# Kernel optimization log

Hardware: AMD Instinct MI355X
Metric: run time of the kernel (lower is better)

## Reference

```python
import jax, jax.numpy as jnp
import numpy as np

DT = 1e-3
TAU_SYN_INV = 200.0  # norse default 1/5e-3
TAU_MEM_INV = 100.0  # norse default 1/1e-2
A_PLUS, A_MINUS = 0.004, 0.003


def conv(x, w):
    return jax.lax.conv_general_dilated(x, w, (1, 1), 'VALID',
                                        dimension_numbers=('NCHW', 'OIHW', 'NCHW'))


def maxpool(x, k, s):
    return jax.lax.reduce_window(x, -jnp.inf, jax.lax.max, (1, 1, k, k), (1, 1, s, s), 'VALID')


def iaf(v_state, inp, v_th):
    # integrate-and-fire: accumulate, spike at threshold, reset to 0
    v = v_state + inp
    z = (v >= v_th).astype(inp.dtype)
    return z, v * (1.0 - z), v  # spikes, new state, pre-reset potential


def stdp(s_pre, w, v, mask, threshold):
    # get_update_index: per-output-channel winner (max masked potential, batch-avg)
    # STDP_learning: multiplicative STDP dw = (a+*pre - a-*(1-pre)) * w * (1-w) at winner, gated by v>threshold
    C, k = w.shape[0], w.shape[-1]
    pm = jnp.mean(v * mask, axis=0)                 # [C,H,W]
    Wd = pm.shape[-1]
    flat = pm.reshape(C, -1)
    idx = jnp.argmax(flat, axis=1)
    maxval = jnp.max(flat, axis=1)
    h, ww = idx // Wd, idx % Wd
    pre = jnp.mean(s_pre, axis=0)                   # [Cin,Hp,Wp]
    patch = lambda hc, wc: jax.lax.dynamic_slice(pre, (0, hc, wc), (pre.shape[0], k, k))
    patches = jax.vmap(patch)(h, ww)                # [C,Cin,k,k]
    fired = (maxval >= threshold)[:, None, None, None]
    dw = jnp.where(fired, A_PLUS * patches - A_MINUS * (1.0 - patches), 0.0) * w * (1.0 - w)
    return jnp.clip(w + dw, 0.0, 1.0)


def setup_inputs() -> dict:
    key = jax.random.key(0)
    ks = jax.random.split(key, 8)
    T, B = 30, 32
    x = jax.random.uniform(ks[0], (T, B, 1, 240, 160), dtype=jnp.float32)
    w1 = 0.8 + 0.05 * jax.random.normal(ks[1], (4, 1, 5, 5), dtype=jnp.float32)
    w2 = 0.8 + 0.05 * jax.random.normal(ks[2], (20, 4, 16, 16), dtype=jnp.float32)
    w3 = 0.8 + 0.05 * jax.random.normal(ks[3], (10, 20, 5, 5), dtype=jnp.float32)
    fc1_w = jax.random.normal(ks[4], (50, B * 10), dtype=jnp.float32) / np.sqrt(B * 10)
    fc1_b = jnp.zeros((50,), jnp.float32)
    out_w = jax.random.normal(ks[5], (10, 50), dtype=jnp.float32) / np.sqrt(50)
    out_b = jnp.zeros((10,), jnp.float32)
    return {'x': x, 'w1': w1, 'w2': w2, 'w3': w3,
            'fc1_w': fc1_w, 'fc1_b': fc1_b, 'out_w': out_w, 'out_b': out_b}


def reference(x, w1, w2, w3, fc1_w, fc1_b, out_w, out_b):
    T, B = x.shape[0], x.shape[1]
    v1 = jnp.zeros((B, 4, 236, 156), x.dtype)
    v2 = jnp.zeros((B, 20, 24, 10), x.dtype)
    v3 = jnp.zeros((B, 10, 8, 1), x.dtype)
    m1, m2, m3 = jnp.ones_like(v1), jnp.ones_like(v2), jnp.ones_like(v3)
    lv = jnp.zeros((1, 10), x.dtype)
    li = jnp.zeros((1, 10), x.dtype)

    def step(carry, xt):
        w1, w2, w3, v1, v2, v3, m1, m2, m3, lv, li = carry
        # layer 1: conv -> IAF -> lateral inhibition (once fired, inhibited)
        z2, v1n, v1p = iaf(v1, conv(xt, w1), 10.0)
        z2 = z2 * m1; m1n = m1 * (1.0 - z2)
        z3 = maxpool(z2, 7, 6)
        z5, v2n, v2p = iaf(v2, conv(z3, w2), 60.0)
        z5 = z5 * m2; m2n = m2 * (1.0 - z5)
        z6 = maxpool(z5, 2, 2)
        z8, v3n, v3p = iaf(v3, conv(z6, w3), 2.0)
        z8 = z8 * m3; m3n = m3 * (1.0 - z8)
        z9 = jnp.max(z8, axis=(2, 3))                       # global max pool -> [B,10]
        # STDP weight updates (torch runs these under no_grad)
        w1n = jax.lax.stop_gradient(stdp(xt, w1, v1p, m1n, 10.0))
        w2n = jax.lax.stop_gradient(stdp(z3, w2, v2p, m2n, 60.0))
        w3n = jax.lax.stop_gradient(stdp(z6, w3, v3p, m3n, 2.0))
        # readout: z9.view(-1, B*10) -> [1, B*10] -> fc1 -> relu -> LILinearCell
        feat = jax.lax.stop_gradient(z9).reshape(1, -1)
        h = jax.nn.relu(feat @ fc1_w.T + fc1_b)
        i_dec = li * (1.0 - DT * TAU_SYN_INV)
        v_new = lv + DT * TAU_MEM_INV * (i_dec - lv)
        i_new = i_dec + h @ out_w.T + out_b
        volt = jnp.broadcast_to(v_new, (B, 10))
        return (w1n, w2n, w3n, v1n, v2n, v3n, m1n, m2n, m3n, v_new, i_new), volt

    carry0 = (w1, w2, w3, v1, v2, v3, m1, m2, m3, lv, li)
    carry, volts = jax.lax.scan(step, carry0, x)
    return volts, carry[0], carry[1]
```

## Files before the change

### kernel.cpp

```cpp
#include <hip/hip_runtime.h>


#define T_STEPS 30
#define BATCH   32
#define H_IN    240
#define W_IN    160
#define C1      4
#define H1      236
#define W1O     156
#define H3      39
#define W3      25
#define C2      20
#define H2      24
#define W2O     10
#define C3      10
#define H8      8

#define N1PB   (C1*H1*W1O)
#define N_V1   (BATCH*N1PB)
#define N_V2PB (C2*H2*W2O)
#define N_V2   (BATCH*N_V2PB)
#define Z3PB   (C1*H3*W3)
#define N_Z3   (BATCH*Z3PB)
#define N_POOL (BATCH*H3*W3)
#define N_FEAT (BATCH*C3)

#define NTHR 256

__device__ __forceinline__ float wave64_sum_dpp(float s) {
  s += __int_as_float(__builtin_amdgcn_update_dpp(0, __float_as_int(s), 0x111, 0xf, 0xf, true));
  s += __int_as_float(__builtin_amdgcn_update_dpp(0, __float_as_int(s), 0x112, 0xf, 0xf, true));
  s += __int_as_float(__builtin_amdgcn_update_dpp(0, __float_as_int(s), 0x114, 0xf, 0xf, true));
  s += __int_as_float(__builtin_amdgcn_update_dpp(0, __float_as_int(s), 0x118, 0xf, 0xf, true));
  s += __int_as_float(__builtin_amdgcn_update_dpp(0, __float_as_int(s), 0x142, 0xa, 0xf, true));
  s += __int_as_float(__builtin_amdgcn_update_dpp(0, __float_as_int(s), 0x143, 0xc, 0xf, true));
  return s;
}

__global__ __launch_bounds__(NTHR) void k1_conv1pool(
    const float* __restrict__ x, const float* __restrict__ w1,
    unsigned char* __restrict__ z3, int* alive_flag)
{
  __shared__ float s_w1[C1*25];
  for (int i = threadIdx.x; i < C1*25; i += NTHR) s_w1[i] = w1[i];
  __syncthreads();
  int it = blockIdx.x*NTHR + threadIdx.x;
  if (it == 0) *alive_flag = 0;
  int o = it >> 3, q = it & 7;
  int px = o % W3; int tt = o / W3;
  int py = tt % H3; int b = tt / H3;
  unsigned mask = 0;
  if (q < 7) {
    const float* xb = x + (size_t)b*H_IN*W_IN;
    int ybase = py*6 + q;
    float acc[C1][7];
    #pragma unroll
    for (int c = 0; c < C1; ++c)
      #pragma unroll
      for (int wx = 0; wx < 7; ++wx) acc[c][wx] = 0.f;
    #pragma unroll
    for (int i = 0; i < 5; ++i) {
      const float* xp = xb + (size_t)(ybase + i)*W_IN + px*6;
      float xr[11];
      #pragma unroll
      for (int k = 0; k < 11; ++k) xr[k] = xp[k];
      #pragma unroll
      for (int j = 0; j < 5; ++j) {
        float w0 = s_w1[ 0 + i*5 + j];
        float w1v = s_w1[25 + i*5 + j];
        float w2v = s_w1[50 + i*5 + j];
        float w3v = s_w1[75 + i*5 + j];
        #pragma unroll
        for (int wx = 0; wx < 7; ++wx) {
          float xv = xr[wx + j];
          acc[0][wx] = fmaf(xv, w0,  acc[0][wx]);
          acc[1][wx] = fmaf(xv, w1v, acc[1][wx]);
          acc[2][wx] = fmaf(xv, w2v, acc[2][wx]);
          acc[3][wx] = fmaf(xv, w3v, acc[3][wx]);
        }
      }
    }
    #pragma unroll
    for (int c = 0; c < C1; ++c)
      #pragma unroll
      for (int wx = 0; wx < 7; ++wx)
        mask |= (acc[c][wx] >= 10.f) ? (1u << c) : 0u;
  }
  mask |= __shfl_xor(mask, 1, 64);
  mask |= __shfl_xor(mask, 2, 64);
  mask |= __shfl_xor(mask, 4, 64);
  if (q == 0 && o < N_POOL) {
    unsigned char* zp = z3 + (size_t)b*Z3PB + py*W3 + px;
    zp[0]        =  mask       & 1;
    zp[H3*W3]    = (mask >> 1) & 1;
    zp[2*H3*W3]  = (mask >> 2) & 1;
    zp[3*H3*W3]  = (mask >> 3) & 1;
  }
}

__global__ __launch_bounds__(NTHR) void k2_conv2(
    const unsigned char* __restrict__ z3, const float* __restrict__ w2,
    unsigned char* __restrict__ z5, int* alive_flag)
{
  __shared__ unsigned s_mask[C1*H3];
  __shared__ int s_any[4];
  const int b = blockIdx.x & 31;
  const int c = blockIdx.x >> 5;
  const int tid = threadIdx.x;
  const int lane = tid & 63;
  const int wv = tid >> 6;
  if (tid < C1*H3) {
    const unsigned char* rp = z3 + (size_t)b*Z3PB + tid*W3;
    unsigned m = 0;
    #pragma unroll
    for (int k = 0; k < W3; ++k) m |= (rp[k] ? 1u : 0u) << k;
    s_mask[tid] = m;
  }
  float wreg[16];
  {
    const float4* wp = (const float4*)(w2 + (size_t)c*C1*256 + lane*16);
    #pragma unroll
    for (int k = 0; k < 4; ++k) {
      float4 v = wp[k];
      wreg[4*k+0] = v.x; wreg[4*k+1] = v.y; wreg[4*k+2] = v.z; wreg[4*k+3] = v.w;
    }
  }
  __syncthreads();
  const int mrow = (lane >> 4)*H3 + (lane & 15);
  int surv = 0;
  for (int oy = wv*6; oy < wv*6 + 6; ++oy) {
    unsigned mw = s_mask[mrow + oy];
    #pragma unroll
    for (int ox = 0; ox < 10; ++ox) {
      unsigned mm = mw >> ox;
      float s = 0.f;
      #pragma unroll
      for (int j = 0; j < 16; ++j)
        s += (mm & (1u << j)) ? wreg[j] : 0.f;
      s = wave64_sum_dpp(s);
      if (lane == 63) {
        unsigned char sp = (s >= 60.0f) ? 1 : 0;
        z5[b*N_V2PB + c*(H2*W2O) + oy*W2O + ox] = sp;
        surv |= (sp == 0);
      }
    }
  }
  if (lane == 63) s_any[wv] = surv;
  __syncthreads();
  if (tid == 0 && (s_any[0] | s_any[1] | s_any[2] | s_any[3]))
    *alive_flag = 1;
}

__global__ __launch_bounds__(NTHR) void k3_conv3(
    const unsigned char* __restrict__ z5, const float* __restrict__ w3,
    float* __restrict__ z9)
{
  const int b = blockIdx.x, tid = threadIdx.x;
  __shared__ unsigned int s_z5w[N_V2PB/4];
  __shared__ unsigned char s_z8[C3*H8];
  const unsigned int* zsrc = (const unsigned int*)(z5 + (size_t)b*N_V2PB);
  for (int i = tid; i < N_V2PB/4; i += NTHR) s_z5w[i] = zsrc[i];
  __syncthreads();
  const unsigned char* sz = (const unsigned char*)s_z5w;
  for (int it = tid; it < C3*H8*4; it += NTHR) {
    int o = it >> 2, g = it & 3;
    int c3 = o >> 3, oy = o & 7;
    float s = 0.f;
    for (int ci = g*5; ci < g*5 + 5; ++ci) {
      const unsigned char* zp = sz + ci*H2*W2O;
      const float* wp = w3 + ((size_t)c3*C2 + ci)*25;
      #pragma unroll
      for (int i = 0; i < 5; ++i) {
        const unsigned char* r0 = zp + (2*(oy + i))*W2O;
        const unsigned char* r1 = r0 + W2O;
        #pragma unroll
        for (int j = 0; j < 5; ++j) {
          unsigned char zv = r0[2*j] | r0[2*j+1] | r1[2*j] | r1[2*j+1];
          s = fmaf((float)zv, wp[i*5 + j], s);
        }
      }
    }
    s += __shfl_xor(s, 1, 64);
    s += __shfl_xor(s, 2, 64);
    if (g == 0) s_z8[o] = (s >= 2.0f) ? 1 : 0;
  }
  __syncthreads();
  if (tid < C3) {
    unsigned char r = 0;
    #pragma unroll
    for (int k = 0; k < H8; ++k) r |= s_z8[tid*H8 + k];
    z9[b*C3 + tid] = (float)r;
  }
}

__global__ __launch_bounds__(NTHR) void f1_fallback(
    const float* __restrict__ x,  const float* __restrict__ w1,
    const float* __restrict__ w2, const float* __restrict__ w3,
    float* v1, unsigned char* m1, unsigned char* z2,
    float* __restrict__ z9, const int* alive_flag)
{
  if (*alive_flag == 0) return;
  const int b = blockIdx.x, tid = threadIdx.x;
  __shared__ float s_w1[C1*25];
  __shared__ unsigned char s_z3[Z3PB];
  __shared__ float s_v2[N_V2PB];
  __shared__ unsigned char s_m2[N_V2PB], s_z5[N_V2PB];
  __shared__ float s_v3[C3*H8];
  __shared__ unsigned char s_m3[C3*H8], s_z8[C3*H8];

  for (int i = tid; i < C1*25; i += NTHR) s_w1[i] = w1[i];
  float* v1b = v1 + (size_t)b*N1PB;
  unsigned char* m1b = m1 + (size_t)b*N1PB;
  unsigned char* z2b = z2 + (size_t)b*N1PB;
  __syncthreads();

  const float* x0 = x + (size_t)b*H_IN*W_IN;
  for (int idx = tid; idx < N1PB; idx += NTHR) {
    int xw = idx % W1O; int r = idx / W1O;
    int y  = r % H1;    int c = r / H1;
    const float* xp = x0 + (size_t)y*W_IN + xw;
    const float* wp = s_w1 + c*25;
    float s = 0.f;
    #pragma unroll
    for (int i = 0; i < 5; ++i)
      #pragma unroll
      for (int j = 0; j < 5; ++j) s = fmaf(xp[i*W_IN + j], wp[i*5 + j], s);
    bool z = (s >= 10.0f);
    v1b[idx] = z ? 0.f : s;
    m1b[idx] = z ? 0 : 1;
  }
  __syncthreads();
  for (int i = tid; i < Z3PB; i += NTHR) {
    int px = i % W3; int r = i / W3;
    int py = r % H3; int cc = r / H3;
    const unsigned char* p = m1b + ((size_t)cc*H1 + py*6)*W1O + px*6;
    unsigned char rr = 0;
    #pragma unroll
    for (int ii = 0; ii < 7; ++ii)
      #pragma unroll
      for (int jj = 0; jj < 7; ++jj) rr |= (p[ii*W1O + jj] == 0) ? 1 : 0;
    s_z3[i] = rr;
  }
  __syncthreads();
  for (int o = tid; o < N_V2PB; o += NTHR) {
    int c  = o / (H2*W2O);
    int r  = o - c*(H2*W2O);
    int oy = r / W2O, ox = r - (r/W2O)*W2O;
    const float* wb = w2 + (size_t)c*C1*256;
    float s = 0.f;
    for (int ci = 0; ci < C1; ++ci)
      for (int i = 0; i < 16; ++i) {
        const unsigned char* ip = s_z3 + (ci*H3 + oy + i)*W3 + ox;
        const float* wp = wb + ci*256 + i*16;
        #pragma unroll
        for (int j = 0; j < 16; ++j) s = fmaf((float)ip[j], wp[j], s);
      }
    bool z = (s >= 60.0f);
    s_v2[o] = z ? 0.f : s;
    s_m2[o] = z ? 0 : 1;
    s_z5[o] = z ? 1 : 0;
  }
  __syncthreads();
  for (int o = tid; o < C3*H8; o += NTHR) {
    int c3 = o >> 3, oy = o & 7;
    float s = 0.f;
    for (int ci = 0; ci < C2; ++ci) {
      const unsigned char* zp = s_z5 + ci*H2*W2O;
      const float* wp = w3 + ((size_t)c3*C2 + ci)*25;
      #pragma unroll
      for (int i = 0; i < 5; ++i) {
        const unsigned char* r0 = zp + (2*(oy + i))*W2O;
        const unsigned char* r1 = r0 + W2O;
        #pragma unroll
        for (int j = 0; j < 5; ++j) {
          unsigned char zv = r0[2*j] | r0[2*j+1] | r1[2*j] | r1[2*j+1];
          s = fmaf((float)zv, wp[i*5 + j], s);
        }
      }
    }
    bool z = (s >= 2.0f);
    s_v3[o] = z ? 0.f : s;
    s_m3[o] = z ? 0 : 1;
    s_z8[o] = z ? 1 : 0;
  }
  __syncthreads();
  if (tid < C3) {
    unsigned char r = 0;
    #pragma unroll
    for (int k = 0; k < H8; ++k) r |= s_z8[tid*H8 + k];
    z9[b*C3 + tid] = (float)r;
  }
  __syncthreads();

  for (int t = 1; t < T_STEPS; ++t) {
    const float* xt = x + ((size_t)t*BATCH + b)*H_IN*W_IN;
    for (int idx = tid; idx < N1PB; idx += NTHR) {
      int xw = idx % W1O; int r = idx / W1O;
      int y  = r % H1;    int c = r / H1;
      const float* xp = xt + (size_t)y*W_IN + xw;
      const float* wp = s_w1 + c*25;
      float s = 0.f;
      #pragma unroll
      for (int i = 0; i < 5; ++i)
        #pragma unroll
        for (int j = 0; j < 5; ++j) s = fmaf(xp[i*W_IN + j], wp[i*5 + j], s);
      float v = v1b[idx] + s;
      bool  z = (v >= 10.0f);
      v1b[idx] = z ? 0.f : v;
      unsigned char m = m1b[idx];
      z2b[idx] = (z && m) ? 1 : 0;
      m1b[idx] = (m && !z) ? 1 : 0;
    }
    __syncthreads();
    for (int i = tid; i < Z3PB; i += NTHR) {
      int px = i % W3; int r = i / W3;
      int py = r % H3; int c = r / H3;
      const unsigned char* p = z2b + ((size_t)c*H1 + py*6)*W1O + px*6;
      unsigned char rr = 0;
      #pragma unroll
      for (int ii = 0; ii < 7; ++ii)
        #pragma unroll
        for (int jj = 0; jj < 7; ++jj) rr |= p[ii*W1O + jj];
      s_z3[i] = rr;
    }
    __syncthreads();
    for (int o = tid; o < N_V2PB; o += NTHR) {
      int c  = o / (H2*W2O);
      int r  = o - c*(H2*W2O);
      int oy = r / W2O, ox = r - (r/W2O)*W2O;
      const float* wb = w2 + (size_t)c*C1*256;
      float s = 0.f;
      for (int ci = 0; ci < C1; ++ci)
        for (int i = 0; i < 16; ++i) {
          const unsigned char* ip = s_z3 + (ci*H3 + oy + i)*W3 + ox;
          const float* wp = wb + ci*256 + i*16;
          #pragma unroll
          for (int j = 0; j < 16; ++j) s = fmaf((float)ip[j], wp[j], s);
        }
      float v = s_v2[o] + s;
      bool  z = (v >= 60.0f);
      s_v2[o] = z ? 0.f : v;
      unsigned char m = s_m2[o];
      s_z5[o] = (z && m) ? 1 : 0;
      s_m2[o] = (m && !z) ? 1 : 0;
    }
    __syncthreads();
    for (int o = tid; o < C3*H8; o += NTHR) {
      int c3 = o >> 3, oy = o & 7;
      float s = 0.f;
      for (int ci = 0; ci < C2; ++ci) {
        const unsigned char* zp = s_z5 + ci*H2*W2O;
        const float* wp = w3 + ((size_t)c3*C2 + ci)*25;
        #pragma unroll
        for (int i = 0; i < 5; ++i) {
          const unsigned char* r0 = zp + (2*(oy + i))*W2O;
          const unsigned char* r1 = r0 + W2O;
          #pragma unroll
          for (int j = 0; j < 5; ++j) {
            unsigned char zv = r0[2*j] | r0[2*j+1] | r1[2*j] | r1[2*j+1];
            s = fmaf((float)zv, wp[i*5 + j], s);
          }
        }
      }
      float v = s_v3[o] + s;
      bool  z = (v >= 2.0f);
      s_v3[o] = z ? 0.f : v;
      unsigned char m = s_m3[o];
      s_z8[o] = (z && m) ? 1 : 0;
      s_m3[o] = (m && !z) ? 1 : 0;
    }
    __syncthreads();
    if (tid < C3) {
      unsigned char r = 0;
      #pragma unroll
      for (int k = 0; k < H8; ++k) r |= s_z8[tid*H8 + k];
      z9[(size_t)t*N_FEAT + b*C3 + tid] = (float)r;
    }
    __syncthreads();
  }
}

__global__ __launch_bounds__(NTHR) void f2_head(
    const float* __restrict__ z9,
    const float* __restrict__ fc1_w, const float* __restrict__ fc1_b,
    const float* __restrict__ out_w, const float* __restrict__ out_b,
    const float* __restrict__ w1,    const float* __restrict__ w2,
    float* __restrict__ out, const int* alive_flag)
{
  const int tid = threadIdx.x;
  const int gid = blockIdx.x*NTHR + tid;
  const int gsz = gridDim.x*NTHR;
  float* out_w1 = out + T_STEPS*N_FEAT;
  float* out_w2 = out_w1 + C1*25;
  for (int i = gid; i < C1*25;     i += gsz) out_w1[i] = fminf(fmaxf(w1[i], 0.f), 1.f);
  for (int i = gid; i < C2*C1*256; i += gsz) out_w2[i] = fminf(fmaxf(w2[i], 0.f), 1.f);
  if (blockIdx.x != 0) return;

  __shared__ float s_feat[N_FEAT], s_h[64], s_li[10], s_lv[10];
  __shared__ float s_tail[T_STEPS*10];
  if (tid < 10) { s_li[tid] = 0.f; s_lv[tid] = 0.f; }
  __syncthreads();
  const bool alive = (*alive_flag != 0);
  const int tmax = alive ? T_STEPS : 1;

  for (int t = 0; t < tmax; ++t) {
    for (int i = tid; i < N_FEAT; i += NTHR) s_feat[i] = z9[(size_t)t*N_FEAT + i];
    __syncthreads();
    {
      int o = tid >> 2, q = tid & 3;
      if (o < 50) {
        const float* wr = fc1_w + (size_t)o*N_FEAT + q*80;
        const float* fr = s_feat + q*80;
        float s = 0.f;
        for (int j = 0; j < 80; ++j) s = fmaf(fr[j], wr[j], s);
        s += __shfl_xor(s, 1, 64);
        s += __shfl_xor(s, 2, 64);
        if (q == 0) s_h[o] = fmaxf(s + fc1_b[o], 0.f);
      }
    }
    __syncthreads();
    if (tid < 10) {
      float idec = s_li[tid]*0.8f;
      float vnew = s_lv[tid] + 0.1f*(idec - s_lv[tid]);
      float acc = idec + out_b[tid];
      for (int k = 0; k < 50; ++k) acc = fmaf(s_h[k], out_w[tid*50 + k], acc);
      s_li[tid] = acc;
      s_lv[tid] = vnew;
    }
    __syncthreads();
    float* vt = out + (size_t)t*N_FEAT;
    for (int i = tid; i < N_FEAT; i += NTHR) vt[i] = s_lv[i % 10];
    __syncthreads();
  }

  if (!alive) {
    if (tid < 50) s_h[tid] = fmaxf(fc1_b[tid], 0.f);
    __syncthreads();
    if (tid < 10) {
      float c = out_b[tid];
      for (int k = 0; k < 50; ++k) c = fmaf(s_h[k], out_w[tid*50 + k], c);
      float li = s_li[tid], lv = s_lv[tid];
      for (int tt = 1; tt < T_STEPS; ++tt) {
        float idec = li*0.8f;
        lv = lv + 0.1f*(idec - lv);
        li = idec + c;
        s_tail[(tt - 1)*10 + tid] = lv;
      }
    }
    __syncthreads();
    int nrem = (T_STEPS - 1)*N_FEAT;
    float* vt = out + (size_t)N_FEAT;
    for (int i = tid; i < nrem; i += NTHR)
      vt[i] = s_tail[(i/N_FEAT)*10 + (i % 10)];
  }
}

extern "C" void kernel_launch(void* const* d_in, const int* in_sizes, int n_in,
                              void* d_out, int out_size, void* d_ws, size_t ws_size,
                              hipStream_t stream) {
  const float* x      = (const float*)d_in[0];
  const float* w1     = (const float*)d_in[1];
  const float* w2     = (const float*)d_in[2];
  const float* w3     = (const float*)d_in[3];
  const float* fc1_w  = (const float*)d_in[4];
  const float* fc1_b  = (const float*)d_in[5];
  const float* out_w  = (const float*)d_in[6];
  const float* out_b  = (const float*)d_in[7];
  float* out = (float*)d_out;

  char* p = (char*)d_ws;
  float* v1 = (float*)p;                  p += (size_t)N_V1*4;
  float* z9 = (float*)p;                  p += (size_t)T_STEPS*N_FEAT*4;
  int* alive_flag = (int*)p;              p += 4;
  p += 60;
  unsigned char* m1 = (unsigned char*)p;  p += N_V1;
  unsigned char* z2 = (unsigned char*)p;  p += N_V1;
  unsigned char* z3 = (unsigned char*)p;  p += N_Z3;
  unsigned char* z5 = (unsigned char*)p;  p += N_V2;

  k1_conv1pool<<<975, NTHR, 0, stream>>>(x, w1, z3, alive_flag);
  k2_conv2<<<C2*BATCH, NTHR, 0, stream>>>(z3, w2, z5, alive_flag);
  k3_conv3<<<BATCH, NTHR, 0, stream>>>(z5, w3, z9);
  f1_fallback<<<BATCH, NTHR, 0, stream>>>(x, w1, w2, w3,
                                          v1, m1, z2, z9, alive_flag);
  f2_head<<<64, NTHR, 0, stream>>>(z9, fc1_w, fc1_b, out_w, out_b,
                                   w1, w2, out, alive_flag);
}
```

Baseline: 50.20 us.

## Fuse conv3 into fallback kernel, split conv2 rows across blocks, move weight copy

Merges the conv3 kernel into the fallback kernel so one launch disappears, and moves the clamped weight output copy from the head kernel into the conv1 kernel so the head can run as a single block. Conv2 is re-gridded six times wider: each wave handles one output row and builds its bitmask straight from global memory, with no shared memory or block barriers. This cuts launch count and serial per-block work in exchange for redundant weight loads across more blocks and more atomic-free flag writes.

```diff
diff --git a/kernel.cpp b/kernel.cpp
--- a/kernel.cpp
+++ b/kernel.cpp
@@ -26,6 +26,7 @@
 #define N_FEAT (BATCH*C3)
 
 #define NTHR 256
+#define K1_BLOCKS 975
 
 __device__ __forceinline__ float wave64_sum_dpp(float s) {
   s += __int_as_float(__builtin_amdgcn_update_dpp(0, __float_as_int(s), 0x111, 0xf, 0xf, true));
@@ -39,13 +40,18 @@
 
 __global__ __launch_bounds__(NTHR) void k1_conv1pool(
     const float* __restrict__ x, const float* __restrict__ w1,
-    unsigned char* __restrict__ z3, int* alive_flag)
+    const float* __restrict__ w2,
+    unsigned char* __restrict__ z3, int* alive_flag,
+    float* __restrict__ out_w1, float* __restrict__ out_w2)
 {
   __shared__ float s_w1[C1*25];
   for (int i = threadIdx.x; i < C1*25; i += NTHR) s_w1[i] = w1[i];
   __syncthreads();
   int it = blockIdx.x*NTHR + threadIdx.x;
+  const int gsz = K1_BLOCKS*NTHR;
   if (it == 0) *alive_flag = 0;
+  for (int i = it; i < C1*25;     i += gsz) out_w1[i] = fminf(fmaxf(w1[i], 0.f), 1.f);
+  for (int i = it; i < C2*C1*256; i += gsz) out_w2[i] = fminf(fmaxf(w2[i], 0.f), 1.f);
   int o = it >> 3, q = it & 7;
   int px = o % W3; int tt = o / W3;
   int py = tt % H3; int b = tt / H3;
@@ -102,104 +108,55 @@
     const unsigned char* __restrict__ z3, const float* __restrict__ w2,
     unsigned char* __restrict__ z5, int* alive_flag)
 {
-  __shared__ unsigned s_mask[C1*H3];
-  __shared__ int s_any[4];
-  const int b = blockIdx.x & 31;
-  const int c = blockIdx.x >> 5;
+  const int b  = blockIdx.x & 31;
+  const int cg = blockIdx.x >> 5;
+  const int c  = cg / 6;
+  const int g  = cg - c*6;
   const int tid = threadIdx.x;
   const int lane = tid & 63;
   const int wv = tid >> 6;
-  if (tid < C1*H3) {
-    const unsigned char* rp = z3 + (size_t)b*Z3PB + tid*W3;
-    unsigned m = 0;
-    #pragma unroll
-    for (int k = 0; k < W3; ++k) m |= (rp[k] ? 1u : 0u) << k;
-    s_mask[tid] = m;
-  }
+  const int oy = g*4 + wv;
+  const int ci = lane >> 4, ii = lane & 15;
   float wreg[16];
   {
-    const float4* wp = (const float4*)(w2 + (size_t)c*C1*256 + lane*16);
+    const float4* wp = (const float4*)(w2 + ((size_t)c*C1 + ci)*256 + ii*16);
     #pragma unroll
     for (int k = 0; k < 4; ++k) {
       float4 v = wp[k];
       wreg[4*k+0] = v.x; wreg[4*k+1] = v.y; wreg[4*k+2] = v.z; wreg[4*k+3] = v.w;
     }
   }
-  __syncthreads();
-  const int mrow = (lane >> 4)*H3 + (lane & 15);
+  unsigned mw = 0;
+  {
+    const unsigned char* rp = z3 + (size_t)b*Z3PB + (ci*H3 + oy + ii)*W3;
+    #pragma unroll
+    for (int k = 0; k < W3; ++k) mw |= (rp[k] ? 1u : 0u) << k;
+  }
   int surv = 0;
-  for (int oy = wv*6; oy < wv*6 + 6; ++oy) {
-    unsigned mw = s_mask[mrow + oy];
-    #pragma unroll
-    for (int ox = 0; ox < 10; ++ox) {
-      unsigned mm = mw >> ox;
-      float s = 0.f;
-      #pragma unroll
-      for (int j = 0; j < 16; ++j)
-        s += (mm & (1u << j)) ? wreg[j] : 0.f;
-      s = wave64_sum_dpp(s);
-      if (lane == 63) {
-        unsigned char sp = (s >= 60.0f) ? 1 : 0;
-        z5[b*N_V2PB + c*(H2*W2O) + oy*W2O + ox] = sp;
-        surv |= (sp == 0);
-      }
-    }
-  }
-  if (lane == 63) s_any[wv] = surv;
-  __syncthreads();
-  if (tid == 0 && (s_any[0] | s_any[1] | s_any[2] | s_any[3]))
-    *alive_flag = 1;
-}
-
-__global__ __launch_bounds__(NTHR) void k3_conv3(
-    const unsigned char* __restrict__ z5, const float* __restrict__ w3,
-    float* __restrict__ z9)
-{
-  const int b = blockIdx.x, tid = threadIdx.x;
-  __shared__ unsigned int s_z5w[N_V2PB/4];
-  __shared__ unsigned char s_z8[C3*H8];
-  const unsigned int* zsrc = (const unsigned int*)(z5 + (size_t)b*N_V2PB);
-  for (int i = tid; i < N_V2PB/4; i += NTHR) s_z5w[i] = zsrc[i];
-  __syncthreads();
-  const unsigned char* sz = (const unsigned char*)s_z5w;
-  for (int it = tid; it < C3*H8*4; it += NTHR) {
-    int o = it >> 2, g = it & 3;
-    int c3 = o >> 3, oy = o & 7;
+  #pragma unroll
+  for (int ox = 0; ox < 10; ++ox) {
+    unsigned mm = mw >> ox;
     float s = 0.f;
-    for (int ci = g*5; ci < g*5 + 5; ++ci) {
-      const unsigned char* zp = sz + ci*H2*W2O;
-      const float* wp = w3 + ((size_t)c3*C2 + ci)*25;
-      #pragma unroll
-      for (int i = 0; i < 5; ++i) {
-        const unsigned char* r0 = zp + (2*(oy + i))*W2O;
-        const unsigned char* r1 = r0 + W2O;
-        #pragma unroll
-        for (int j = 0; j < 5; ++j) {
-          unsigned char zv = r0[2*j] | r0[2*j+1] | r1[2*j] | r1[2*j+1];
-          s = fmaf((float)zv, wp[i*5 + j], s);
-        }
-      }
-    }
-    s += __shfl_xor(s, 1, 64);
-    s += __shfl_xor(s, 2, 64);
-    if (g == 0) s_z8[o] = (s >= 2.0f) ? 1 : 0;
-  }
-  __syncthreads();
-  if (tid < C3) {
-    unsigned char r = 0;
-    #pragma unroll
-    for (int k = 0; k < H8; ++k) r |= s_z8[tid*H8 + k];
-    z9[b*C3 + tid] = (float)r;
-  }
-}
-
-__global__ __launch_bounds__(NTHR) void f1_fallback(
+    #pragma unroll
+    for (int j = 0; j < 16; ++j)
+      s += (mm & (1u << j)) ? wreg[j] : 0.f;
+    s = wave64_sum_dpp(s);
+    if (lane == 63) {
+      unsigned char sp = (s >= 60.0f) ? 1 : 0;
+      z5[b*N_V2PB + c*(H2*W2O) + oy*W2O + ox] = sp;
+      surv |= (sp == 0);
+    }
+  }
+  if (lane == 63 && surv) *alive_flag = 1;
+}
+
+__global__ __launch_bounds__(NTHR) void k3f1(
+    const unsigned char* __restrict__ z5g, const float* __restrict__ w3,
     const float* __restrict__ x,  const float* __restrict__ w1,
-    const float* __restrict__ w2, const float* __restrict__ w3,
+    const float* __restrict__ w2,
     float* v1, unsigned char* m1, unsigned char* z2,
     float* __restrict__ z9, const int* alive_flag)
 {
-  if (*alive_flag == 0) return;
   const int b = blockIdx.x, tid = threadIdx.x;
   __shared__ float s_w1[C1*25];
   __shared__ unsigned char s_z3[Z3PB];
@@ -208,6 +165,44 @@
   __shared__ float s_v3[C3*H8];
   __shared__ unsigned char s_m3[C3*H8], s_z8[C3*H8];
 
+  {
+    const unsigned int* zsrc = (const unsigned int*)(z5g + (size_t)b*N_V2PB);
+    unsigned int* dst = (unsigned int*)s_z5;
+    for (int i = tid; i < N_V2PB/4; i += NTHR) dst[i] = zsrc[i];
+  }
+  __syncthreads();
+  for (int it = tid; it < C3*H8*4; it += NTHR) {
+    int o = it >> 2, g = it & 3;
+    int c3 = o >> 3, oy = o & 7;
+    float s = 0.f;
+    for (int ci = g*5; ci < g*5 + 5; ++ci) {
+      const unsigned char* zp = s_z5 + ci*H2*W2O;
+      const float* wp = w3 + ((size_t)c3*C2 + ci)*25;
+      #pragma unroll
+      for (int i = 0; i < 5; ++i) {
+        const unsigned char* r0 = zp + (2*(oy + i))*W2O;
+        const unsigned char* r1 = r0 + W2O;
+        #pragma unroll
+        for (int j = 0; j < 5; ++j) {
+          unsigned char zv = r0[2*j] | r0[2*j+1] | r1[2*j] | r1[2*j+1];
+          s = fmaf((float)zv, wp[i*5 + j], s);
+        }
+      }
+    }
+    s += __shfl_xor(s, 1, 64);
+    s += __shfl_xor(s, 2, 64);
+    if (g == 0) s_z8[o] = (s >= 2.0f) ? 1 : 0;
+  }
+  __syncthreads();
+  if (tid < C3) {
+    unsigned char r = 0;
+    #pragma unroll
+    for (int k = 0; k < H8; ++k) r |= s_z8[tid*H8 + k];
+    z9[b*C3 + tid] = (float)r;
+  }
+
+  if (*alive_flag == 0) return;
+  __syncthreads();
   for (int i = tid; i < C1*25; i += NTHR) s_w1[i] = w1[i];
   float* v1b = v1 + (size_t)b*N1PB;
   unsigned char* m1b = m1 + (size_t)b*N1PB;
@@ -384,18 +379,9 @@
     const float* __restrict__ z9,
     const float* __restrict__ fc1_w, const float* __restrict__ fc1_b,
     const float* __restrict__ out_w, const float* __restrict__ out_b,
-    const float* __restrict__ w1,    const float* __restrict__ w2,
     float* __restrict__ out, const int* alive_flag)
 {
   const int tid = threadIdx.x;
-  const int gid = blockIdx.x*NTHR + tid;
-  const int gsz = gridDim.x*NTHR;
-  float* out_w1 = out + T_STEPS*N_FEAT;
-  float* out_w2 = out_w1 + C1*25;
-  for (int i = gid; i < C1*25;     i += gsz) out_w1[i] = fminf(fmaxf(w1[i], 0.f), 1.f);
-  for (int i = gid; i < C2*C1*256; i += gsz) out_w2[i] = fminf(fmaxf(w2[i], 0.f), 1.f);
-  if (blockIdx.x != 0) return;
-
   __shared__ float s_feat[N_FEAT], s_h[64], s_li[10], s_lv[10];
   __shared__ float s_tail[T_STEPS*10];
   if (tid < 10) { s_li[tid] = 0.f; s_lv[tid] = 0.f; }
@@ -467,6 +453,8 @@
   const float* out_w  = (const float*)d_in[6];
   const float* out_b  = (const float*)d_in[7];
   float* out = (float*)d_out;
+  float* out_w1 = out + T_STEPS*N_FEAT;
+  float* out_w2 = out_w1 + C1*25;
 
   char* p = (char*)d_ws;
   float* v1 = (float*)p;                  p += (size_t)N_V1*4;
@@ -478,11 +466,11 @@
   unsigned char* z3 = (unsigned char*)p;  p += N_Z3;
   unsigned char* z5 = (unsigned char*)p;  p += N_V2;
 
-  k1_conv1pool<<<975, NTHR, 0, stream>>>(x, w1, z3, alive_flag);
-  k2_conv2<<<C2*BATCH, NTHR, 0, stream>>>(z3, w2, z5, alive_flag);
-  k3_conv3<<<BATCH, NTHR, 0, stream>>>(z5, w3, z9);
-  f1_fallback<<<BATCH, NTHR, 0, stream>>>(x, w1, w2, w3,
-                                          v1, m1, z2, z9, alive_flag);
-  f2_head<<<64, NTHR, 0, stream>>>(z9, fc1_w, fc1_b, out_w, out_b,
-                                   w1, w2, out, alive_flag);
-}
+  k1_conv1pool<<<K1_BLOCKS, NTHR, 0, stream>>>(x, w1, w2, z3, alive_flag,
+                                               out_w1, out_w2);
+  k2_conv2<<<BATCH*C2*6, NTHR, 0, stream>>>(z3, w2, z5, alive_flag);
+  k3f1<<<BATCH, NTHR, 0, stream>>>(z5, w3, x, w1, w2,
+                                   v1, m1, z2, z9, alive_flag);
+  f2_head<<<1, NTHR, 0, stream>>>(z9, fc1_w, fc1_b, out_w, out_b,
+                                  out, alive_flag);
+}
```

Measured after the change: 46.71 us. 6.9% less time.
